# Kernel tuning notes

Hardware: AMD Instinct MI355X
Metric: run time of the kernel (lower is better)

The kernel has to match this reference:

```python
import jax, jax.numpy as jnp
import numpy as np

B, N, D, H = 4, 1024, 256, 8  # batch, seq, in_dim(=per-head qkv_dim), n_heads


def setup_inputs() -> dict:
    key = jax.random.key(0)
    k1, k2, k3 = jax.random.split(key, 3)
    x = jax.random.normal(k1, (B, N, D), dtype=jnp.float32)
    Wqkv = jax.random.normal(k2, (D, 3 * D * H), dtype=jnp.float32) * 0.02
    bqkv = jnp.zeros((3 * D * H,), dtype=jnp.float32)
    W0 = jax.random.normal(k3, (D * H, D), dtype=jnp.float32) * 0.02
    b0 = jnp.zeros((D,), dtype=jnp.float32)
    return {"x": x, "Wqkv": Wqkv, "bqkv": bqkv, "W0": W0, "b0": b0}


def reference(x, Wqkv, bqkv, W0, b0):
    b, n, d = x.shape
    h = Wqkv.shape[1] // (3 * d)
    qkv = x @ Wqkv + bqkv                      # [b, n, 3*d*h]
    # Faithful to torch: raw row-major reinterpretation of the buffer.
    q, k, v = jnp.reshape(qkv, (3, b, n, d, h))
    score = jnp.einsum('bnqh,btqh->bnth', q, k) * (d ** -0.5)  # [b, n, n, h]
    attn = jax.nn.softmax(score, axis=1)       # softmax over query axis (dim=1), as in source
    # einsum 'bnnh,bnqh->bnqh' = diagonal of attn times v (faithful to source)
    av = jnp.einsum('bnnh,bnqh->bnqh', attn, v)  # [b, n, d, h]
    out = av.reshape(b, n, d * h) @ W0 + b0    # [b, n, d]
    return out
```

## Files before the change

### kernel.cpp

```cpp
#include <hip/hip_runtime.h>


#define SEGSZ 8388608

typedef short v8s __attribute__((ext_vector_type(8)));
typedef float v4f __attribute__((ext_vector_type(4)));

__device__ __forceinline__ ushort f2bf(float v) {
  union { float f; unsigned u; } x; x.f = v;
  const unsigned r = x.u + 0x7fff + ((x.u >> 16) & 1);
  return (ushort)(r >> 16);
}
__device__ __forceinline__ float bf2f(ushort v) {
  union { unsigned u; float f; } x; x.u = ((unsigned)v) << 16;
  return x.f;
}

#define GLOAD_LDS16(g, l)                                            \
  __builtin_amdgcn_global_load_lds(                                  \
      (const __attribute__((address_space(1))) void*)(g),            \
      (__attribute__((address_space(3))) void*)(l), 16, 0, 0)

__global__ __launch_bounds__(256) void prep(
    const float* __restrict__ X, const float* __restrict__ Wqkv,
    const float* __restrict__ W0, ushort* __restrict__ xb,
    ushort* __restrict__ whT, ushort* __restrict__ w0T) {
  __shared__ float T[64][65];
  const int tid = threadIdx.x;
  int bid = blockIdx.x;

  if (bid < 1024) {
    const size_t i = ((size_t)bid * 256 + tid) * 4;
    const float4 v = *(const float4*)&X[i];
    ushort4 hv = {f2bf(v.x), f2bf(v.y), f2bf(v.z), f2bf(v.w)};
    *(ushort4*)&xb[i] = hv;
    return;
  }
  bid -= 1024;
  if (bid < 384) {
    const int n0 = (bid % 96) * 64;
    const int k0 = (bid / 96) * 64;
    {
      const int row = tid >> 2;
      const int c0 = (tid & 3) * 16;
#pragma unroll
      for (int j = 0; j < 16; j += 4) {
        const float4 v = *(const float4*)&Wqkv[(size_t)(k0 + row) * 6144 + n0 + c0 + j];
        T[row][c0 + j + 0] = v.x; T[row][c0 + j + 1] = v.y;
        T[row][c0 + j + 2] = v.z; T[row][c0 + j + 3] = v.w;
      }
    }
    __syncthreads();
    {
      const int nn = tid >> 2;
      const int kk0 = (tid & 3) * 16;
      const int n = n0 + nn;
      const int seg = n >> 11, h = n & 7, d = (n & 2047) >> 3;
      const int p = seg * 2048 + h * 256 + d;
      ushort hv[16];
#pragma unroll
      for (int j = 0; j < 16; ++j) hv[j] = f2bf(T[kk0 + j][nn]);
      const size_t base = (size_t)p * 256 + k0 + kk0;
#pragma unroll
      for (int j = 0; j < 16; j += 8) *(v8s*)&whT[base + j] = *(v8s*)&hv[j];
    }
    return;
  }
  bid -= 384;
  {
    const int e0 = (bid & 3) * 64;
    const int k0 = (bid >> 2) * 64;
    {
      const int row = tid >> 2;
      const int c0 = (tid & 3) * 16;
#pragma unroll
      for (int j = 0; j < 16; j += 4) {
        const float4 v = *(const float4*)&W0[(size_t)(k0 + row) * 256 + e0 + c0 + j];
        T[row][c0 + j + 0] = v.x; T[row][c0 + j + 1] = v.y;
        T[row][c0 + j + 2] = v.z; T[row][c0 + j + 3] = v.w;
      }
    }
    __syncthreads();
    {
      const int ee = tid >> 2;
      const int kk0 = (tid & 3) * 16;
#pragma unroll
      for (int j = 0; j < 16; ++j) {
        const int k = k0 + kk0 + j;
        const int d = k >> 3, h = k & 7;
        w0T[(size_t)(e0 + ee) * 2048 + h * 256 + d] = f2bf(T[kk0 + j][ee]);
      }
    }
  }
}

__global__ __launch_bounds__(256) void qkv_mfma(
    const ushort* __restrict__ xb, const ushort* __restrict__ whT,
    const float* __restrict__ bias, ushort* __restrict__ qkvb) {
  __shared__ ushort As[128 * 32];
  __shared__ ushort Bh[128 * 32];
  const int tid = threadIdx.x;
  const int wave = tid >> 6, lane = tid & 63;
  const int quad = lane >> 4, l15 = lane & 15;
  const int c0 = blockIdx.x * 128;
  const int r0 = blockIdx.y * 128;
  const int wr = (wave >> 1) * 64;
  const int wc = (wave & 1) * 64;

  v4f acc[4][4] = {};

  for (int d0 = 0; d0 < 256; d0 += 32) {
#pragma unroll
    for (int half = 0; half < 2; ++half) {
      const int rr = wave * 32 + half * 16;
      const int row = rr + (lane >> 2);
      const int gcol = d0 + (lane & 3) * 8;
      GLOAD_LDS16(xb + (size_t)(r0 + row) * 256 + gcol, &As[rr * 32]);
      GLOAD_LDS16(whT + (size_t)(c0 + row) * 256 + gcol, &Bh[rr * 32]);
    }
    __syncthreads();

    v8s aF[4], bF[4];
#pragma unroll
    for (int i = 0; i < 4; ++i) {
      aF[i] = *(const v8s*)&As[(wr + i * 16 + l15) * 32 + quad * 8];
      bF[i] = *(const v8s*)&Bh[(wc + i * 16 + l15) * 32 + quad * 8];
    }
#pragma unroll
    for (int ri = 0; ri < 4; ++ri)
#pragma unroll
      for (int ci = 0; ci < 4; ++ci)
        acc[ri][ci] = __builtin_amdgcn_mfma_f32_16x16x32_bf16(
            aF[ri], bF[ci], acc[ri][ci], 0, 0, 0);
    __syncthreads();
  }

#pragma unroll
  for (int ci = 0; ci < 4; ++ci) {
    const int c = c0 + wc + ci * 16 + l15;
    const int cseg = c >> 11;
    const int h = (c & 2047) >> 8;
    const int d = c & 255;
    const float bv = bias[cseg * 2048 + d * 8 + h];
#pragma unroll
    for (int ri = 0; ri < 4; ++ri)
#pragma unroll
      for (int rg = 0; rg < 4; ++rg) {
        const int r = r0 + wr + ri * 16 + quad * 4 + rg;
        const int g = r * 3 + cseg;
        const int seg = g >> 12;
        const int tok = g & 4095;
        float val = acc[ri][ci][rg] + bv;
        if (seg == 0) val *= 0.0625f;
        qkvb[(size_t)seg * SEGSZ + (size_t)tok * 2048 + h * 256 + d] = f2bf(val);
      }
  }
}

__global__ __launch_bounds__(256) void scores_mfma(
    const ushort* __restrict__ qkvb, float* __restrict__ pl,
    float* __restrict__ sd_ws) {
  __shared__ ushort Qs[128 * 32];
  __shared__ ushort Ks[128 * 32];
  __shared__ float redL[2][2][64];

  const int tid = threadIdx.x;
  const int wave = tid >> 6, lane = tid & 63;
  const int quad = lane >> 4, l15 = lane & 15;
  const int bh = blockIdx.z * 8 + blockIdx.x;
  const int tile = blockIdx.y;
  const int tt0 = (tile >> 3) * 128;
  const int nn0 = (tile & 7) * 128;
  const int b = bh >> 3, h = bh & 7;
  const ushort* Qg = qkvb + (size_t)b * 1024 * 2048 + h * 256;
  const ushort* Kg = Qg + SEGSZ;

  const int wr = (wave >> 1) * 64;
  const int wc = (wave & 1) * 64;

  v4f acc[4][4] = {};

  for (int d0 = 0; d0 < 256; d0 += 32) {
#pragma unroll
    for (int half = 0; half < 2; ++half) {
      const int rr = wave * 32 + half * 16;
      const int row = rr + (lane >> 2);
      const int gcol = d0 + (lane & 3) * 8;
      GLOAD_LDS16(Qg + (size_t)(nn0 + row) * 2048 + gcol, &Qs[rr * 32]);
      GLOAD_LDS16(Kg + (size_t)(tt0 + row) * 2048 + gcol, &Ks[rr * 32]);
    }
    __syncthreads();

    v8s aF[4], bF[4];
#pragma unroll
    for (int i = 0; i < 4; ++i) {
      aF[i] = *(const v8s*)&Qs[(wr + i * 16 + l15) * 32 + quad * 8];
      bF[i] = *(const v8s*)&Ks[(wc + i * 16 + l15) * 32 + quad * 8];
    }
#pragma unroll
    for (int ri = 0; ri < 4; ++ri)
#pragma unroll
      for (int ci = 0; ci < 4; ++ci)
        acc[ri][ci] =
            __builtin_amdgcn_mfma_f32_16x16x32_bf16(aF[ri], bF[ci], acc[ri][ci], 0, 0, 0);
    __syncthreads();
  }

  float lsum[4];
#pragma unroll
  for (int ci = 0; ci < 4; ++ci) {
    float s = 0.f;
#pragma unroll
    for (int ri = 0; ri < 4; ++ri)
#pragma unroll
      for (int rg = 0; rg < 4; ++rg) s += __expf(acc[ri][ci][rg]);
    s += __shfl_xor(s, 16, 64);
    s += __shfl_xor(s, 32, 64);
    lsum[ci] = s;
  }
  if (quad == 0) {
#pragma unroll
    for (int ci = 0; ci < 4; ++ci)
      redL[wave & 1][wave >> 1][ci * 16 + l15] = lsum[ci];
  }
  __syncthreads();
  if ((wave >> 1) == 0 && quad == 0) {
#pragma unroll
    for (int ci = 0; ci < 4; ++ci) {
      const int t = tt0 + (wave & 1) * 64 + ci * 16 + l15;
      const float l = lsum[ci] + redL[wave & 1][1][ci * 16 + l15];
      pl[((size_t)bh * 1024 + t) * 8 + (tile & 7)] = l;
    }
  }

  if (tt0 == nn0 && (wave == 0 || wave == 3) && quad == (l15 >> 2)) {
#pragma unroll
    for (int ri = 0; ri < 4; ++ri) {
      const int t = tt0 + (wave & 1) * 64 + ri * 16 + l15;
      sd_ws[(size_t)bh * 1024 + t] = acc[ri][ri][l15 & 3];
    }
  }
}

template <bool ATOMIC>
__global__ __launch_bounds__(256) void av_mfma(
    const ushort* __restrict__ vb, const ushort* __restrict__ w0T,
    const float* __restrict__ pl, const float* __restrict__ sd,
    ushort* __restrict__ partial, float* __restrict__ out) {
  __shared__ ushort As[128 * 32];
  __shared__ ushort Bs[128 * 32];
  __shared__ float diagS[128];
  const int tid = threadIdx.x;
  const int wave = tid >> 6, lane = tid & 63;
  const int quad = lane >> 4, l15 = lane & 15;
  const int e0 = blockIdx.x * 128;
  const int tok0 = blockIdx.y * 128;
  const int h = blockIdx.z;
  const int kbase = h * 256;
  const int wr = (wave >> 1) * 64;
  const int wc = (wave & 1) * 64;

  if (tid < 128) {
    const int bh = (tok0 >> 10) * 8 + h;
    const int t = (tok0 & 1023) + tid;
    const size_t base = ((size_t)bh * 1024 + t) * 8;
    float l = 0.f;
#pragma unroll
    for (int c = 0; c < 8; ++c) l += pl[base + c];
    diagS[tid] = __expf(sd[(size_t)bh * 1024 + t]) / l;
  }

  v4f acc[4][4] = {};

  for (int d0 = 0; d0 < 256; d0 += 32) {
#pragma unroll
    for (int half = 0; half < 2; ++half) {
      const int rr = wave * 32 + half * 16;
      const int row = rr + (lane >> 2);
      const int gcol = kbase + d0 + (lane & 3) * 8;
      GLOAD_LDS16(vb + (size_t)(tok0 + row) * 2048 + gcol, &As[rr * 32]);
      GLOAD_LDS16(w0T + (size_t)(e0 + row) * 2048 + gcol, &Bs[rr * 32]);
    }
    __syncthreads();

    v8s aF[4], bF[4];
#pragma unroll
    for (int i = 0; i < 4; ++i) {
      aF[i] = *(const v8s*)&As[(wr + i * 16 + l15) * 32 + quad * 8];
      bF[i] = *(const v8s*)&Bs[(wc + i * 16 + l15) * 32 + quad * 8];
    }
#pragma unroll
    for (int ri = 0; ri < 4; ++ri)
#pragma unroll
      for (int ci = 0; ci < 4; ++ci)
        acc[ri][ci] =
            __builtin_amdgcn_mfma_f32_16x16x32_bf16(aF[ri], bF[ci], acc[ri][ci], 0, 0, 0);
    __syncthreads();
  }

#pragma unroll
  for (int ri = 0; ri < 4; ++ri)
#pragma unroll
    for (int rg = 0; rg < 4; ++rg) {
      const int lrow = wr + ri * 16 + quad * 4 + rg;
      const int tok = tok0 + lrow;
      const float dg = diagS[lrow];
#pragma unroll
      for (int ci = 0; ci < 4; ++ci) {
        const int e = e0 + wc + ci * 16 + l15;
        const float val = acc[ri][ci][rg] * dg;
        if (ATOMIC)
          atomicAdd(&out[(size_t)tok * 256 + e], val);
        else
          partial[(size_t)h * 1048576 + (size_t)tok * 256 + e] = f2bf(val);
      }
    }
}

__global__ void init_out(const float* __restrict__ b0, float* __restrict__ out) {
  const int i = blockIdx.x * 256 + threadIdx.x;
  const int e0 = (i & 63) << 2;
  *(float4*)&out[(size_t)i * 4] = *(const float4*)&b0[e0];
}

__global__ void reduce_out(const ushort* __restrict__ partial,
                           const float* __restrict__ b0, float* __restrict__ out) {
  const int i = blockIdx.x * 256 + threadIdx.x;
  const int e0 = (i & 63) << 2;
  float4 a = *(const float4*)&b0[e0];
#pragma unroll
  for (int h = 0; h < 8; ++h) {
    const ushort4 p = *(const ushort4*)&partial[(size_t)h * 1048576 + (size_t)i * 4];
    a.x += bf2f(p.x); a.y += bf2f(p.y); a.z += bf2f(p.z); a.w += bf2f(p.w);
  }
  *(float4*)&out[(size_t)i * 4] = a;
}

extern "C" void kernel_launch(void* const* d_in, const int* in_sizes, int n_in,
                              void* d_out, int out_size, void* d_ws, size_t ws_size,
                              hipStream_t stream) {
  const float* x    = (const float*)d_in[0];
  const float* Wqkv = (const float*)d_in[1];
  const float* bqkv = (const float*)d_in[2];
  const float* W0   = (const float*)d_in[3];
  const float* b0   = (const float*)d_in[4];
  float* out = (float*)d_out;

  float*  pl   = (float*)d_ws;
  float*  sd   = pl + 262144;
  ushort* qkvb = (ushort*)(sd + 32768);
  ushort* xb   = qkvb + 3 * (size_t)SEGSZ;
  ushort* whT  = xb + 1048576;
  ushort* w0T  = whT + 1572864;
  ushort* partial = w0T + 524288;

  ushort* vb = qkvb + 2 * (size_t)SEGSZ;

  const size_t need_base =
      (size_t)(262144 + 32768) * 4 + (size_t)SEGSZ * 3 * 2 +
      (size_t)(1048576 + 1572864 + 524288) * 2;
  const bool full = ws_size >= need_base + (size_t)8 * 1048576 * 2;

  prep<<<1536, 256, 0, stream>>>(x, Wqkv, W0, xb, whT, w0T);
  qkv_mfma<<<dim3(48, 32), 256, 0, stream>>>(xb, whT, bqkv, qkvb);
  scores_mfma<<<dim3(8, 64, 4), 256, 0, stream>>>(qkvb, pl, sd);
  if (full) {
    av_mfma<false><<<dim3(2, 32, 8), 256, 0, stream>>>(vb, w0T, pl, sd, partial, out);
    reduce_out<<<1024, 256, 0, stream>>>(partial, b0, out);
  } else {
    init_out<<<1024, 256, 0, stream>>>(b0, out);
    av_mfma<true><<<dim3(2, 32, 8), 256, 0, stream>>>(vb, w0T, pl, sd, nullptr, out);
  }
}
```

Before: 141.9 us.

## Fuse scores and V·W0 GEMMs into one launch, defer diagonal scaling to reduce

The V·W0 per-head product does not depend on the softmax diagonal, so it is moved into the same launch as the score GEMM (blocks 2048+ compute V·W0 partials unscaled). The diagonal softmax weight is then computed and applied in reduce_out instead. This removes one kernel launch and lets the two independent GEMMs share the GPU concurrently, filling idle CUs. The cost is storing unscaled partials in bf16 and applying the scale afterwards, which changes rounding slightly. There is also a stray label in the fallback path.

```diff
diff --git a/kernel.cpp b/kernel.cpp
--- a/kernel.cpp
+++ b/kernel.cpp
@@ -157,96 +157,146 @@
   }
 }
 
-__global__ __launch_bounds__(256) void scores_mfma(
-    const ushort* __restrict__ qkvb, float* __restrict__ pl,
-    float* __restrict__ sd_ws) {
-  __shared__ ushort Qs[128 * 32];
-  __shared__ ushort Ks[128 * 32];
+__global__ __launch_bounds__(256) void mid_fused(
+    const ushort* __restrict__ qkvb, const ushort* __restrict__ w0T,
+    float* __restrict__ pl, float* __restrict__ sd_ws,
+    ushort* __restrict__ partial) {
+  __shared__ ushort S1[128 * 32];
+  __shared__ ushort S2[128 * 32];
   __shared__ float redL[2][2][64];
 
   const int tid = threadIdx.x;
   const int wave = tid >> 6, lane = tid & 63;
   const int quad = lane >> 4, l15 = lane & 15;
-  const int bh = blockIdx.z * 8 + blockIdx.x;
-  const int tile = blockIdx.y;
-  const int tt0 = (tile >> 3) * 128;
-  const int nn0 = (tile & 7) * 128;
-  const int b = bh >> 3, h = bh & 7;
-  const ushort* Qg = qkvb + (size_t)b * 1024 * 2048 + h * 256;
-  const ushort* Kg = Qg + SEGSZ;
-
   const int wr = (wave >> 1) * 64;
   const int wc = (wave & 1) * 64;
+  const int id = blockIdx.x;
 
   v4f acc[4][4] = {};
 
-  for (int d0 = 0; d0 < 256; d0 += 32) {
-#pragma unroll
-    for (int half = 0; half < 2; ++half) {
-      const int rr = wave * 32 + half * 16;
-      const int row = rr + (lane >> 2);
-      const int gcol = d0 + (lane & 3) * 8;
-      GLOAD_LDS16(Qg + (size_t)(nn0 + row) * 2048 + gcol, &Qs[rr * 32]);
-      GLOAD_LDS16(Kg + (size_t)(tt0 + row) * 2048 + gcol, &Ks[rr * 32]);
-    }
-    __syncthreads();
-
-    v8s aF[4], bF[4];
-#pragma unroll
-    for (int i = 0; i < 4; ++i) {
-      aF[i] = *(const v8s*)&Qs[(wr + i * 16 + l15) * 32 + quad * 8];
-      bF[i] = *(const v8s*)&Ks[(wc + i * 16 + l15) * 32 + quad * 8];
-    }
+  if (id < 2048) {
+    const int bh = (id >> 9) * 8 + (id & 7);
+    const int tile = (id >> 3) & 63;
+    const int tt0 = (tile >> 3) * 128;
+    const int nn0 = (tile & 7) * 128;
+    const int b = bh >> 3, h = bh & 7;
+    const ushort* Qg = qkvb + (size_t)b * 1024 * 2048 + h * 256;
+    const ushort* Kg = Qg + SEGSZ;
+
+    for (int d0 = 0; d0 < 256; d0 += 32) {
+#pragma unroll
+      for (int half = 0; half < 2; ++half) {
+        const int rr = wave * 32 + half * 16;
+        const int row = rr + (lane >> 2);
+        const int gcol = d0 + (lane & 3) * 8;
+        GLOAD_LDS16(Qg + (size_t)(nn0 + row) * 2048 + gcol, &S1[rr * 32]);
+        GLOAD_LDS16(Kg + (size_t)(tt0 + row) * 2048 + gcol, &S2[rr * 32]);
+      }
+      __syncthreads();
+
+      v8s aF[4], bF[4];
+#pragma unroll
+      for (int i = 0; i < 4; ++i) {
+        aF[i] = *(const v8s*)&S1[(wr + i * 16 + l15) * 32 + quad * 8];
+        bF[i] = *(const v8s*)&S2[(wc + i * 16 + l15) * 32 + quad * 8];
+      }
+#pragma unroll
+      for (int ri = 0; ri < 4; ++ri)
+#pragma unroll
+        for (int ci = 0; ci < 4; ++ci)
+          acc[ri][ci] = __builtin_amdgcn_mfma_f32_16x16x32_bf16(
+              aF[ri], bF[ci], acc[ri][ci], 0, 0, 0);
+      __syncthreads();
+    }
+
+    float lsum[4];
+#pragma unroll
+    for (int ci = 0; ci < 4; ++ci) {
+      float s = 0.f;
+#pragma unroll
+      for (int ri = 0; ri < 4; ++ri)
+#pragma unroll
+        for (int rg = 0; rg < 4; ++rg) s += __expf(acc[ri][ci][rg]);
+      s += __shfl_xor(s, 16, 64);
+      s += __shfl_xor(s, 32, 64);
+      lsum[ci] = s;
+    }
+    if (quad == 0) {
+#pragma unroll
+      for (int ci = 0; ci < 4; ++ci)
+        redL[wave & 1][wave >> 1][ci * 16 + l15] = lsum[ci];
+    }
+    __syncthreads();
+    if ((wave >> 1) == 0 && quad == 0) {
+#pragma unroll
+      for (int ci = 0; ci < 4; ++ci) {
+        const int t = tt0 + (wave & 1) * 64 + ci * 16 + l15;
+        const float l = lsum[ci] + redL[wave & 1][1][ci * 16 + l15];
+        pl[((size_t)bh * 1024 + t) * 8 + (tile & 7)] = l;
+      }
+    }
+
+    if (tt0 == nn0 && (wave == 0 || wave == 3) && quad == (l15 >> 2)) {
+#pragma unroll
+      for (int ri = 0; ri < 4; ++ri) {
+        const int t = tt0 + (wave & 1) * 64 + ri * 16 + l15;
+        sd_ws[(size_t)bh * 1024 + t] = acc[ri][ri][l15 & 3];
+      }
+    }
+  } else {
+    const int j = id - 2048;
+    const int e0 = (j & 1) * 128;
+    const int tok0 = ((j >> 1) & 31) * 128;
+    const int h = j >> 6;
+    const int kbase = h * 256;
+    const ushort* vb = qkvb + 2 * (size_t)SEGSZ;
+
+    for (int d0 = 0; d0 < 256; d0 += 32) {
+#pragma unroll
+      for (int half = 0; half < 2; ++half) {
+        const int rr = wave * 32 + half * 16;
+        const int row = rr + (lane >> 2);
+        const int gcol = kbase + d0 + (lane & 3) * 8;
+        GLOAD_LDS16(vb + (size_t)(tok0 + row) * 2048 + gcol, &S1[rr * 32]);
+        GLOAD_LDS16(w0T + (size_t)(e0 + row) * 2048 + gcol, &S2[rr * 32]);
+      }
+      __syncthreads();
+
+      v8s aF[4], bF[4];
+#pragma unroll
+      for (int i = 0; i < 4; ++i) {
+        aF[i] = *(const v8s*)&S1[(wr + i * 16 + l15) * 32 + quad * 8];
+        bF[i] = *(const v8s*)&S2[(wc + i * 16 + l15) * 32 + quad * 8];
+      }
+#pragma unroll
+      for (int ri = 0; ri < 4; ++ri)
+#pragma unroll
+        for (int ci = 0; ci < 4; ++ci)
+          acc[ri][ci] = __builtin_amdgcn_mfma_f32_16x16x32_bf16(
+              aF[ri], bF[ci], acc[ri][ci], 0, 0, 0);
+      __syncthreads();
+    }
+
 #pragma unroll
     for (int ri = 0; ri < 4; ++ri)
 #pragma unroll
-      for (int ci = 0; ci < 4; ++ci)
-        acc[ri][ci] =
-            __builtin_amdgcn_mfma_f32_16x16x32_bf16(aF[ri], bF[ci], acc[ri][ci], 0, 0, 0);
-    __syncthreads();
-  }
-
-  float lsum[4];
-#pragma unroll
-  for (int ci = 0; ci < 4; ++ci) {
-    float s = 0.f;
-#pragma unroll
-    for (int ri = 0; ri < 4; ++ri)
-#pragma unroll
-      for (int rg = 0; rg < 4; ++rg) s += __expf(acc[ri][ci][rg]);
-    s += __shfl_xor(s, 16, 64);
-    s += __shfl_xor(s, 32, 64);
-    lsum[ci] = s;
-  }
-  if (quad == 0) {
-#pragma unroll
-    for (int ci = 0; ci < 4; ++ci)
-      redL[wave & 1][wave >> 1][ci * 16 + l15] = lsum[ci];
-  }
-  __syncthreads();
-  if ((wave >> 1) == 0 && quad == 0) {
-#pragma unroll
-    for (int ci = 0; ci < 4; ++ci) {
-      const int t = tt0 + (wave & 1) * 64 + ci * 16 + l15;
-      const float l = lsum[ci] + redL[wave & 1][1][ci * 16 + l15];
-      pl[((size_t)bh * 1024 + t) * 8 + (tile & 7)] = l;
-    }
-  }
-
-  if (tt0 == nn0 && (wave == 0 || wave == 3) && quad == (l15 >> 2)) {
-#pragma unroll
-    for (int ri = 0; ri < 4; ++ri) {
-      const int t = tt0 + (wave & 1) * 64 + ri * 16 + l15;
-      sd_ws[(size_t)bh * 1024 + t] = acc[ri][ri][l15 & 3];
-    }
-  }
-}
-
-template <bool ATOMIC>
-__global__ __launch_bounds__(256) void av_mfma(
+      for (int rg = 0; rg < 4; ++rg) {
+        const int lrow = wr + ri * 16 + quad * 4 + rg;
+        const int tok = tok0 + lrow;
+#pragma unroll
+        for (int ci = 0; ci < 4; ++ci) {
+          const int e = e0 + wc + ci * 16 + l15;
+          partial[(size_t)h * 1048576 + (size_t)tok * 256 + e] =
+              f2bf(acc[ri][ci][rg]);
+        }
+      }
+  }
+}
+
+__global__ __launch_bounds__(256) void av_atomic(
     const ushort* __restrict__ vb, const ushort* __restrict__ w0T,
     const float* __restrict__ pl, const float* __restrict__ sd,
-    ushort* __restrict__ partial, float* __restrict__ out) {
+    float* __restrict__ out) {
   __shared__ ushort As[128 * 32];
   __shared__ ushort Bs[128 * 32];
   __shared__ float diagS[128];
@@ -308,11 +358,7 @@
 #pragma unroll
       for (int ci = 0; ci < 4; ++ci) {
         const int e = e0 + wc + ci * 16 + l15;
-        const float val = acc[ri][ci][rg] * dg;
-        if (ATOMIC)
-          atomicAdd(&out[(size_t)tok * 256 + e], val);
-        else
-          partial[(size_t)h * 1048576 + (size_t)tok * 256 + e] = f2bf(val);
+        atomicAdd(&out[(size_t)tok * 256 + e], acc[ri][ci][rg] * dg);
       }
     }
 }
@@ -324,14 +370,33 @@
 }
 
 __global__ void reduce_out(const ushort* __restrict__ partial,
+                           const float* __restrict__ pl,
+                           const float* __restrict__ sd,
                            const float* __restrict__ b0, float* __restrict__ out) {
+  __shared__ float dgS[32];
   const int i = blockIdx.x * 256 + threadIdx.x;
+  const int tbase = blockIdx.x * 4;
+  if (threadIdx.x < 32) {
+    const int tl = threadIdx.x >> 3, h = threadIdx.x & 7;
+    const int tok = tbase + tl;
+    const int bh = (tok >> 10) * 8 + h;
+    const int t = tok & 1023;
+    const size_t base = ((size_t)bh * 1024 + t) * 8;
+    float l = 0.f;
+#pragma unroll
+    for (int c = 0; c < 8; ++c) l += pl[base + c];
+    dgS[threadIdx.x] = __expf(sd[(size_t)bh * 1024 + t]) / l;
+  }
+  __syncthreads();
+  const int tl = threadIdx.x >> 6;
   const int e0 = (i & 63) << 2;
   float4 a = *(const float4*)&b0[e0];
 #pragma unroll
   for (int h = 0; h < 8; ++h) {
+    const float dg = dgS[tl * 8 + h];
     const ushort4 p = *(const ushort4*)&partial[(size_t)h * 1048576 + (size_t)i * 4];
-    a.x += bf2f(p.x); a.y += bf2f(p.y); a.z += bf2f(p.z); a.w += bf2f(p.w);
+    a.x += dg * bf2f(p.x); a.y += dg * bf2f(p.y);
+    a.z += dg * bf2f(p.z); a.w += dg * bf2f(p.w);
   }
   *(float4*)&out[(size_t)i * 4] = a;
 }
@@ -363,12 +428,13 @@
 
   prep<<<1536, 256, 0, stream>>>(x, Wqkv, W0, xb, whT, w0T);
   qkv_mfma<<<dim3(48, 32), 256, 0, stream>>>(xb, whT, bqkv, qkvb);
-  scores_mfma<<<dim3(8, 64, 4), 256, 0, stream>>>(qkvb, pl, sd);
   if (full) {
-    av_mfma<false><<<dim3(2, 32, 8), 256, 0, stream>>>(vb, w0T, pl, sd, partial, out);
-    reduce_out<<<1024, 256, 0, stream>>>(partial, b0, out);
+    mid_fused<<<2560, 256, 0, stream>>>(qkvb, w0T, pl, sd, partial);
+    reduce_out<<<1024, 256, 0, stream>>>(partial, pl, sd, b0, out);
   } else {
+    scores_fallback:
+    mid_fused<<<2048, 256, 0, stream>>>(qkvb, w0T, pl, sd, nullptr);
     init_out<<<1024, 256, 0, stream>>>(b0, out);
-    av_mfma<true><<<dim3(2, 32, 8), 256, 0, stream>>>(vb, w0T, pl, sd, nullptr, out);
-  }
-}
+    av_atomic<<<dim3(2, 32, 8), 256, 0, stream>>>(vb, w0T, pl, sd, out);
+  }
+}
```

Result: faster. 135.2 us (-4.7%).

## Fold V projection into W0 via precomputed Wv·W0 and drop the AV GEMM

Applied to the files above, without the earlier changes.

Precomputes per-segment, per-head products of the V slice of Wqkv with W0 (wyT) plus a bias term (cws) in a new wy_gemm kernel. The output contribution then comes straight from x times wyT inside the QKV GEMM launch, which skips writing the V segment and removes the separate av_mfma GEMM and its V round trip. The diagonal softmax scale and bias correction move into reduce_out. In exchange there is an extra weight-only GEMM each call, a larger combined launch, and the added bf16 rounding from the precomputed weight product. The ws-size fallback path is removed.

```diff
diff --git a/kernel.cpp b/kernel.cpp
--- a/kernel.cpp
+++ b/kernel.cpp
@@ -24,7 +24,8 @@
 __global__ __launch_bounds__(256) void prep(
     const float* __restrict__ X, const float* __restrict__ Wqkv,
     const float* __restrict__ W0, ushort* __restrict__ xb,
-    ushort* __restrict__ whT, ushort* __restrict__ w0T) {
+    ushort* __restrict__ whT, ushort* __restrict__ w0T,
+    ushort* __restrict__ wvP) {
   __shared__ float T[64][65];
   const int tid = threadIdx.x;
   int bid = blockIdx.x;
@@ -67,7 +68,7 @@
     return;
   }
   bid -= 384;
-  {
+  if (bid < 128) {
     const int e0 = (bid & 3) * 64;
     const int k0 = (bid >> 2) * 64;
     {
@@ -91,21 +92,125 @@
         w0T[(size_t)(e0 + ee) * 2048 + h * 256 + d] = f2bf(T[kk0 + j][ee]);
       }
     }
-  }
-}
-
-__global__ __launch_bounds__(256) void qkv_mfma(
+    return;
+  }
+  bid -= 128;
+  {
+#pragma unroll
+    for (int r = 0; r < 4; ++r) {
+      const int f = bid * 4 + r;
+#pragma unroll
+      for (int m = 0; m < 3; ++m) {
+        const int c0 = (tid + 256 * m) * 8;
+        const int s = c0 >> 11, h = (c0 >> 8) & 7, d0 = c0 & 255;
+        ushort hv[8];
+#pragma unroll
+        for (int i = 0; i < 8; ++i)
+          hv[i] = f2bf(Wqkv[(size_t)f * 6144 + s * 2048 + (d0 + i) * 8 + h]);
+        *(v8s*)&wvP[(size_t)f * 6144 + c0] = *(v8s*)&hv[0];
+      }
+    }
+  }
+}
+
+__global__ __launch_bounds__(256) void wy_gemm(
+    const ushort* __restrict__ w0T, const ushort* __restrict__ wvP,
+    const float* __restrict__ bqkv, const float* __restrict__ W0,
+    ushort* __restrict__ wyT, float* __restrict__ cws) {
+  __shared__ ushort As[128 * 32];
+  __shared__ ushort Bs[128 * 32];
+  const int tid = threadIdx.x;
+  const int wave = tid >> 6, lane = tid & 63;
+  const int quad = lane >> 4, l15 = lane & 15;
+  const int et = blockIdx.x >> 1, ft = blockIdx.x & 1;
+  const int h = blockIdx.y, s = blockIdx.z;
+  const int wr = (wave >> 1) * 64;
+  const int wc = (wave & 1) * 64;
+
+  v4f acc[4][4] = {};
+
+  for (int d0 = 0; d0 < 256; d0 += 32) {
+#pragma unroll
+    for (int half = 0; half < 2; ++half) {
+      const int rr = wave * 32 + half * 16;
+      const int row = rr + (lane >> 2);
+      const int gcol = d0 + (lane & 3) * 8;
+      GLOAD_LDS16(w0T + (size_t)(et * 128 + row) * 2048 + h * 256 + gcol,
+                  &As[rr * 32]);
+      GLOAD_LDS16(wvP + (size_t)(ft * 128 + row) * 6144 + s * 2048 + h * 256 + gcol,
+                  &Bs[rr * 32]);
+    }
+    __syncthreads();
+
+    v8s aF[4], bF[4];
+#pragma unroll
+    for (int i = 0; i < 4; ++i) {
+      aF[i] = *(const v8s*)&As[(wr + i * 16 + l15) * 32 + quad * 8];
+      bF[i] = *(const v8s*)&Bs[(wc + i * 16 + l15) * 32 + quad * 8];
+    }
+#pragma unroll
+    for (int ri = 0; ri < 4; ++ri)
+#pragma unroll
+      for (int ci = 0; ci < 4; ++ci)
+        acc[ri][ci] =
+            __builtin_amdgcn_mfma_f32_16x16x32_bf16(aF[ri], bF[ci], acc[ri][ci], 0, 0, 0);
+    __syncthreads();
+  }
+
+#pragma unroll
+  for (int ri = 0; ri < 4; ++ri)
+#pragma unroll
+    for (int rg = 0; rg < 4; ++rg) {
+      const int e = et * 128 + wr + ri * 16 + quad * 4 + rg;
+#pragma unroll
+      for (int ci = 0; ci < 4; ++ci) {
+        const int f = ft * 128 + wc + ci * 16 + l15;
+        wyT[(size_t)(s * 2048 + h * 256 + e) * 256 + f] = f2bf(acc[ri][ci][rg]);
+      }
+    }
+
+  if (blockIdx.x == 0) {
+    const int e = tid;
+    float c = 0.f;
+    for (int d = 0; d < 256; ++d) {
+      const int col = d * 8 + h;
+      c += bqkv[s * 2048 + col] * W0[(size_t)col * 256 + e];
+    }
+    cws[(s * 8 + h) * 256 + e] = c;
+  }
+}
+
+__global__ __launch_bounds__(256) void qkv8(
     const ushort* __restrict__ xb, const ushort* __restrict__ whT,
-    const float* __restrict__ bias, ushort* __restrict__ qkvb) {
+    const ushort* __restrict__ wyT, const float* __restrict__ bias,
+    ushort* __restrict__ qkvb, ushort* __restrict__ partial) {
   __shared__ ushort As[128 * 32];
   __shared__ ushort Bh[128 * 32];
   const int tid = threadIdx.x;
   const int wave = tid >> 6, lane = tid & 63;
   const int quad = lane >> 4, l15 = lane & 15;
-  const int c0 = blockIdx.x * 128;
-  const int r0 = blockIdx.y * 128;
   const int wr = (wave >> 1) * 64;
   const int wc = (wave & 1) * 64;
+  const int id = blockIdx.x;
+
+  const bool is_qkv = id < 1056;
+  int aRow0;
+  const ushort* Bbase;
+  int s = 0, jt = 0, et2 = 0, c0 = 0, r0 = 0;
+  if (is_qkv) {
+    c0 = (id % 48) * 128;
+    r0 = (id / 48) * 128;
+    aRow0 = r0;
+    Bbase = whT + (size_t)c0 * 256;
+  } else {
+    const int j2 = id - 1056;
+    s = j2 / 176;
+    const int rem = j2 % 176;
+    jt = rem / 16;
+    et2 = rem % 16;
+    aRow0 = (2731 - (s == 2)) + jt * 128;
+    Bbase = wyT + (size_t)(s * 2048 + et2 * 128) * 256;
+  }
 
   v4f acc[4][4] = {};
 
@@ -115,8 +220,9 @@
       const int rr = wave * 32 + half * 16;
       const int row = rr + (lane >> 2);
       const int gcol = d0 + (lane & 3) * 8;
-      GLOAD_LDS16(xb + (size_t)(r0 + row) * 256 + gcol, &As[rr * 32]);
-      GLOAD_LDS16(whT + (size_t)(c0 + row) * 256 + gcol, &Bh[rr * 32]);
+      const int ar = min(aRow0 + row, 4095);
+      GLOAD_LDS16(xb + (size_t)ar * 256 + gcol, &As[rr * 32]);
+      GLOAD_LDS16(Bbase + (size_t)row * 256 + gcol, &Bh[rr * 32]);
     }
     __syncthreads();
 
@@ -135,29 +241,50 @@
     __syncthreads();
   }
 
-#pragma unroll
-  for (int ci = 0; ci < 4; ++ci) {
-    const int c = c0 + wc + ci * 16 + l15;
-    const int cseg = c >> 11;
-    const int h = (c & 2047) >> 8;
-    const int d = c & 255;
-    const float bv = bias[cseg * 2048 + d * 8 + h];
+  if (is_qkv) {
+#pragma unroll
+    for (int ci = 0; ci < 4; ++ci) {
+      const int c = c0 + wc + ci * 16 + l15;
+      const int cseg = c >> 11;
+      const int h = (c & 2047) >> 8;
+      const int d = c & 255;
+      const float bv = bias[cseg * 2048 + d * 8 + h];
+#pragma unroll
+      for (int ri = 0; ri < 4; ++ri)
+#pragma unroll
+        for (int rg = 0; rg < 4; ++rg) {
+          const int r = r0 + wr + ri * 16 + quad * 4 + rg;
+          const int g = r * 3 + cseg;
+          const int seg = g >> 12;
+          if (seg == 2) continue;
+          const int tok = g & 4095;
+          float val = acc[ri][ci][rg] + bv;
+          if (seg == 0) val *= 0.0625f;
+          qkvb[(size_t)seg * SEGSZ + (size_t)tok * 2048 + h * 256 + d] = f2bf(val);
+        }
+    }
+  } else {
+    const int cnt = 1365 + (s == 2);
+    const int t0s = (s + 1) % 3;
 #pragma unroll
     for (int ri = 0; ri < 4; ++ri)
 #pragma unroll
       for (int rg = 0; rg < 4; ++rg) {
-        const int r = r0 + wr + ri * 16 + quad * 4 + rg;
-        const int g = r * 3 + cseg;
-        const int seg = g >> 12;
-        const int tok = g & 4095;
-        float val = acc[ri][ci][rg] + bv;
-        if (seg == 0) val *= 0.0625f;
-        qkvb[(size_t)seg * SEGSZ + (size_t)tok * 2048 + h * 256 + d] = f2bf(val);
-      }
-  }
-}
-
-__global__ __launch_bounds__(256) void scores_mfma(
+        const int j = jt * 128 + wr + ri * 16 + quad * 4 + rg;
+        if (j >= cnt) continue;
+        const int tokpp = 3 * j + t0s;
+#pragma unroll
+        for (int ci = 0; ci < 4; ++ci) {
+          const int col = et2 * 128 + wc + ci * 16 + l15;
+          const int h = col >> 8, e = col & 255;
+          partial[(size_t)h * 1048576 + (size_t)tokpp * 256 + e] =
+              f2bf(acc[ri][ci][rg]);
+        }
+      }
+  }
+}
+
+__global__ __launch_bounds__(256) void mid8(
     const ushort* __restrict__ qkvb, float* __restrict__ pl,
     float* __restrict__ sd_ws) {
   __shared__ ushort Qs[128 * 32];
@@ -167,8 +294,9 @@
   const int tid = threadIdx.x;
   const int wave = tid >> 6, lane = tid & 63;
   const int quad = lane >> 4, l15 = lane & 15;
-  const int bh = blockIdx.z * 8 + blockIdx.x;
-  const int tile = blockIdx.y;
+  const int id = blockIdx.x;
+  const int bh = (id >> 9) * 8 + (id & 7);
+  const int tile = (id >> 3) & 63;
   const int tt0 = (tile >> 3) * 128;
   const int nn0 = (tile & 7) * 128;
   const int b = bh >> 3, h = bh & 7;
@@ -242,96 +370,38 @@
   }
 }
 
-template <bool ATOMIC>
-__global__ __launch_bounds__(256) void av_mfma(
-    const ushort* __restrict__ vb, const ushort* __restrict__ w0T,
-    const float* __restrict__ pl, const float* __restrict__ sd,
-    ushort* __restrict__ partial, float* __restrict__ out) {
-  __shared__ ushort As[128 * 32];
-  __shared__ ushort Bs[128 * 32];
-  __shared__ float diagS[128];
-  const int tid = threadIdx.x;
-  const int wave = tid >> 6, lane = tid & 63;
-  const int quad = lane >> 4, l15 = lane & 15;
-  const int e0 = blockIdx.x * 128;
-  const int tok0 = blockIdx.y * 128;
-  const int h = blockIdx.z;
-  const int kbase = h * 256;
-  const int wr = (wave >> 1) * 64;
-  const int wc = (wave & 1) * 64;
-
-  if (tid < 128) {
-    const int bh = (tok0 >> 10) * 8 + h;
-    const int t = (tok0 & 1023) + tid;
+__global__ void reduce_out(const ushort* __restrict__ partial,
+                           const float* __restrict__ pl,
+                           const float* __restrict__ sd,
+                           const float* __restrict__ cws,
+                           const float* __restrict__ b0, float* __restrict__ out) {
+  __shared__ float dgS[32];
+  const int i = blockIdx.x * 256 + threadIdx.x;
+  const int tbase = blockIdx.x * 4;
+  if (threadIdx.x < 32) {
+    const int tl = threadIdx.x >> 3, h = threadIdx.x & 7;
+    const int tok = tbase + tl;
+    const int bh = (tok >> 10) * 8 + h;
+    const int t = tok & 1023;
     const size_t base = ((size_t)bh * 1024 + t) * 8;
     float l = 0.f;
 #pragma unroll
     for (int c = 0; c < 8; ++c) l += pl[base + c];
-    diagS[tid] = __expf(sd[(size_t)bh * 1024 + t]) / l;
-  }
-
-  v4f acc[4][4] = {};
-
-  for (int d0 = 0; d0 < 256; d0 += 32) {
-#pragma unroll
-    for (int half = 0; half < 2; ++half) {
-      const int rr = wave * 32 + half * 16;
-      const int row = rr + (lane >> 2);
-      const int gcol = kbase + d0 + (lane & 3) * 8;
-      GLOAD_LDS16(vb + (size_t)(tok0 + row) * 2048 + gcol, &As[rr * 32]);
-      GLOAD_LDS16(w0T + (size_t)(e0 + row) * 2048 + gcol, &Bs[rr * 32]);
-    }
-    __syncthreads();
-
-    v8s aF[4], bF[4];
-#pragma unroll
-    for (int i = 0; i < 4; ++i) {
-      aF[i] = *(const v8s*)&As[(wr + i * 16 + l15) * 32 + quad * 8];
-      bF[i] = *(const v8s*)&Bs[(wc + i * 16 + l15) * 32 + quad * 8];
-    }
-#pragma unroll
-    for (int ri = 0; ri < 4; ++ri)
-#pragma unroll
-      for (int ci = 0; ci < 4; ++ci)
-        acc[ri][ci] =
-            __builtin_amdgcn_mfma_f32_16x16x32_bf16(aF[ri], bF[ci], acc[ri][ci], 0, 0, 0);
-    __syncthreads();
-  }
-
-#pragma unroll
-  for (int ri = 0; ri < 4; ++ri)
-#pragma unroll
-    for (int rg = 0; rg < 4; ++rg) {
-      const int lrow = wr + ri * 16 + quad * 4 + rg;
-      const int tok = tok0 + lrow;
-      const float dg = diagS[lrow];
-#pragma unroll
-      for (int ci = 0; ci < 4; ++ci) {
-        const int e = e0 + wc + ci * 16 + l15;
-        const float val = acc[ri][ci][rg] * dg;
-        if (ATOMIC)
-          atomicAdd(&out[(size_t)tok * 256 + e], val);
-        else
-          partial[(size_t)h * 1048576 + (size_t)tok * 256 + e] = f2bf(val);
-      }
-    }
-}
-
-__global__ void init_out(const float* __restrict__ b0, float* __restrict__ out) {
-  const int i = blockIdx.x * 256 + threadIdx.x;
-  const int e0 = (i & 63) << 2;
-  *(float4*)&out[(size_t)i * 4] = *(const float4*)&b0[e0];
-}
-
-__global__ void reduce_out(const ushort* __restrict__ partial,
-                           const float* __restrict__ b0, float* __restrict__ out) {
-  const int i = blockIdx.x * 256 + threadIdx.x;
+    dgS[threadIdx.x] = __expf(sd[(size_t)bh * 1024 + t]) / l;
+  }
+  __syncthreads();
+  const int tl = threadIdx.x >> 6;
+  const int tok = tbase + tl;
+  const int s = (tok + 2) % 3;
   const int e0 = (i & 63) << 2;
   float4 a = *(const float4*)&b0[e0];
 #pragma unroll
   for (int h = 0; h < 8; ++h) {
+    const float dg = dgS[tl * 8 + h];
+    const float4 c4 = *(const float4*)&cws[((s * 8 + h) << 8) + e0];
     const ushort4 p = *(const ushort4*)&partial[(size_t)h * 1048576 + (size_t)i * 4];
-    a.x += bf2f(p.x); a.y += bf2f(p.y); a.z += bf2f(p.z); a.w += bf2f(p.w);
+    a.x += dg * (bf2f(p.x) + c4.x); a.y += dg * (bf2f(p.y) + c4.y);
+    a.z += dg * (bf2f(p.z) + c4.z); a.w += dg * (bf2f(p.w) + c4.w);
   }
   *(float4*)&out[(size_t)i * 4] = a;
 }
@@ -353,22 +423,13 @@
   ushort* whT  = xb + 1048576;
   ushort* w0T  = whT + 1572864;
   ushort* partial = w0T + 524288;
-
-  ushort* vb = qkvb + 2 * (size_t)SEGSZ;
-
-  const size_t need_base =
-      (size_t)(262144 + 32768) * 4 + (size_t)SEGSZ * 3 * 2 +
-      (size_t)(1048576 + 1572864 + 524288) * 2;
-  const bool full = ws_size >= need_base + (size_t)8 * 1048576 * 2;
-
-  prep<<<1536, 256, 0, stream>>>(x, Wqkv, W0, xb, whT, w0T);
-  qkv_mfma<<<dim3(48, 32), 256, 0, stream>>>(xb, whT, bqkv, qkvb);
-  scores_mfma<<<dim3(8, 64, 4), 256, 0, stream>>>(qkvb, pl, sd);
-  if (full) {
-    av_mfma<false><<<dim3(2, 32, 8), 256, 0, stream>>>(vb, w0T, pl, sd, partial, out);
-    reduce_out<<<1024, 256, 0, stream>>>(partial, b0, out);
-  } else {
-    init_out<<<1024, 256, 0, stream>>>(b0, out);
-    av_mfma<true><<<dim3(2, 32, 8), 256, 0, stream>>>(vb, w0T, pl, sd, nullptr, out);
-  }
-}
+  ushort* wvP  = partial + 8 * (size_t)1048576;
+  ushort* wyT  = wvP + 1572864;
+  float*  cws  = (float*)(wyT + 1572864);
+
+  prep<<<1600, 256, 0, stream>>>(x, Wqkv, W0, xb, whT, w0T, wvP);
+  wy_gemm<<<dim3(4, 8, 3), 256, 0, stream>>>(w0T, wvP, bqkv, W0, wyT, cws);
+  qkv8<<<1584, 256, 0, stream>>>(xb, whT, wyT, bqkv, qkvb, partial);
+  mid8<<<2048, 256, 0, stream>>>(qkvb, pl, sd);
+  reduce_out<<<1024, 256, 0, stream>>>(partial, pl, sd, cws, b0, out);
+}
```

Result: slower. 177.5 us (+25.1%).
